# Performance work log

Hardware: AMD Instinct MI355X
Metric: run time of the kernel (lower is better)

Reference implementation:

```python
import jax, jax.numpy as jnp
import numpy as np

N_NODES = 100000
N_EDGES = 1600000
IN_DIM = 128
HID = 64
OUT_DIM = 1


def setup_inputs() -> dict:
    key = jax.random.key(0)
    ks = jax.random.split(key, 8)
    x = jax.random.normal(ks[0], (N_NODES, IN_DIM), dtype=jnp.float32)
    edge_index = jax.random.randint(ks[1], (2, N_EDGES), 0, N_NODES, dtype=jnp.int64)
    s_in = 1.0 / np.sqrt(IN_DIM)
    s_h = 1.0 / np.sqrt(HID)
    W_in = jax.random.uniform(ks[2], (IN_DIM, HID), jnp.float32, -s_in, s_in)
    b_in = jax.random.uniform(ks[3], (HID,), jnp.float32, -s_in, s_in)
    W_g = jax.random.uniform(ks[4], (HID, HID), jnp.float32, -s_h, s_h)
    b_g = jnp.zeros((HID,), jnp.float32)
    W_out = jax.random.uniform(ks[5], (HID, OUT_DIM), jnp.float32, -s_h, s_h)
    b_out = jax.random.uniform(ks[6], (OUT_DIM,), jnp.float32, -s_h, s_h)
    return {"x": x, "edge_index": edge_index, "W_in": W_in, "b_in": b_in,
            "W_g": W_g, "b_g": b_g, "W_out": W_out, "b_out": b_out}


def _gcn_conv(h, src, dst, W, b, n_nodes):
    # GCNConv: add self-loops, symmetric normalization, sum aggregation
    loops = jnp.arange(n_nodes, dtype=src.dtype)
    src = jnp.concatenate([src, loops])
    dst = jnp.concatenate([dst, loops])
    hw = h @ W  # [N, out]
    deg = jax.ops.segment_sum(jnp.ones_like(dst, dtype=hw.dtype), dst,
                              num_segments=n_nodes)  # >=1 due to self-loops
    dinv = jax.lax.rsqrt(deg)
    norm = dinv[src] * dinv[dst]  # [E+N]
    msg = hw[src] * norm[:, None]  # gather (memory-bound)
    out = jax.ops.segment_sum(msg, dst, num_segments=n_nodes)  # scatter-add
    return out + b


def reference(x, edge_index, W_in, b_in, W_g, b_g, W_out, b_out):
    n_nodes = x.shape[0]
    h = jax.nn.relu(x @ W_in + b_in)  # input_proj + ReLU (dropout = id in eval)
    # single GCN layer (last layer -> no ReLU/dropout after)
    h = _gcn_conv(h, edge_index[0], edge_index[1], W_g, b_g, n_nodes)
    return h @ W_out + b_out  # [N, 1]
```

## Files before the change

kernel.cpp:

```cpp
#include <hip/hip_runtime.h>

typedef __attribute__((ext_vector_type(8))) short bf16x8;
typedef __attribute__((ext_vector_type(4))) float f32x4;

#define HID 64
#define IN_DIM 128
#define WINB 15
#define WIN (1 << WINB)
#define NGC 4
#define MCH 64
#define SCAN_TPB 1024
#define AWORDS 32768
#define MCH2 64
#define PREP_BLOCKS 8
#define DNODES 64

__device__ __forceinline__ unsigned short f2bf(float f) {
    unsigned u = __builtin_bit_cast(unsigned, f);
    return (unsigned short)((u + 0x7FFFu + ((u >> 16) & 1u)) >> 16);
}

__global__ __launch_bounds__(SCAN_TPB) void k_binA(const int* __restrict__ dst,
                                                   unsigned* __restrict__ partA,
                                                   const float* __restrict__ W_in,
                                                   unsigned short* __restrict__ Wt,
                                                   int E, int chunkA) {
    if ((int)blockIdx.x >= MCH2) {
        int i = (blockIdx.x - MCH2) * SCAN_TPB + threadIdx.x;
        if (i < IN_DIM * HID) Wt[i] = f2bf(W_in[(i & 127) * HID + (i >> 7)]);
        return;
    }

    __shared__ unsigned cnt[AWORDS];
    for (int i = threadIdx.x; i < AWORDS; i += SCAN_TPB) cnt[i] = 0;
    __syncthreads();

    const int e0 = blockIdx.x * chunkA;
    const int e1 = min(E, e0 + chunkA);
    for (int e = e0 + (int)threadIdx.x * 4; e + 3 < e1; e += SCAN_TPB * 4) {
        int4 d4 = *(const int4*)(dst + e);
        atomicAdd(&cnt[(unsigned)d4.x >> 2], 1u << (((unsigned)d4.x & 3u) << 3));
        atomicAdd(&cnt[(unsigned)d4.y >> 2], 1u << (((unsigned)d4.y & 3u) << 3));
        atomicAdd(&cnt[(unsigned)d4.z >> 2], 1u << (((unsigned)d4.z & 3u) << 3));
        atomicAdd(&cnt[(unsigned)d4.w >> 2], 1u << (((unsigned)d4.w & 3u) << 3));
    }
    __syncthreads();

    unsigned* outp = partA + (size_t)blockIdx.x * AWORDS;
    for (int i = threadIdx.x; i < AWORDS; i += SCAN_TPB) outp[i] = cnt[i];
}

__global__ __launch_bounds__(256) void k_dense(const float* __restrict__ x,
                                               const unsigned short* __restrict__ Wt,
                                               const float* __restrict__ b_in,
                                               const float* __restrict__ W_g,
                                               const float* __restrict__ W_out,
                                               const unsigned* __restrict__ partA,
                                               float* __restrict__ dinv,
                                               float* __restrict__ zs,
                                               int N) {
    __shared__ float weff_l[HID];
    __shared__ float bl[HID];
    __shared__ float zp[DNODES];
    __shared__ int   tailp[4][DNODES];

    const int t = threadIdx.x;
    const int row0 = blockIdx.x * DNODES;

    unsigned tw[16];
    int tail_sh;
    {
        const int tn = t & 63;
        const int tq = t >> 6;
        int n = row0 + tn; if (n >= N) n = N - 1;
        tail_sh = (n & 3) << 3;
        const unsigned* base = partA + (n >> 2);
#pragma unroll
        for (int j = 0; j < 16; ++j)
            tw[j] = base[(size_t)(tq * 16 + j) * AWORDS];
    }

    {
        const float* wg = W_g + (t >> 2) * HID + (t & 3) * 16;
        const float* wo = W_out + (t & 3) * 16;
        float s = 0.0f;
#pragma unroll
        for (int p = 0; p < 16; ++p) s = fmaf(wg[p], wo[p], s);
        s += __shfl_xor(s, 1, 64);
        s += __shfl_xor(s, 2, 64);
        if ((t & 3) == 0) weff_l[t >> 2] = s;
        if (t < HID) bl[t] = b_in[t];
    }

    const int w    = __builtin_amdgcn_readfirstlane(t >> 6);
    const int lane = t & 63;

    f32x4 acc[4] = {{0,0,0,0},{0,0,0,0},{0,0,0,0},{0,0,0,0}};
    {
        int grow = row0 + w * 16 + (lane & 15);
        if (grow >= N) grow = N - 1;
        const float* xr = x + (size_t)grow * IN_DIM + (lane >> 4) * 8;
        const unsigned short* wtb = Wt + (size_t)(lane & 15) * IN_DIM + (lane >> 4) * 8;
#pragma unroll
        for (int kk = 0; kk < 4; ++kk) {
            float4 a0 = *(const float4*)(xr + kk * 32);
            float4 a1 = *(const float4*)(xr + kk * 32 + 4);
            bf16x8 af;
            af[0] = (short)f2bf(a0.x); af[1] = (short)f2bf(a0.y);
            af[2] = (short)f2bf(a0.z); af[3] = (short)f2bf(a0.w);
            af[4] = (short)f2bf(a1.x); af[5] = (short)f2bf(a1.y);
            af[6] = (short)f2bf(a1.z); af[7] = (short)f2bf(a1.w);
#pragma unroll
            for (int nf = 0; nf < 4; ++nf) {
                bf16x8 bf = *(const bf16x8*)(wtb + (size_t)(nf * 16) * IN_DIM + kk * 32);
                acc[nf] = __builtin_amdgcn_mfma_f32_16x16x32_bf16(af, bf, acc[nf], 0, 0, 0);
            }
        }
    }
    __syncthreads();

    {
        float p[4] = {0.f, 0.f, 0.f, 0.f};
#pragma unroll
        for (int nf = 0; nf < 4; ++nf) {
            const int col = nf * 16 + (lane & 15);
            const float bc = bl[col], wc = weff_l[col];
#pragma unroll
            for (int r = 0; r < 4; ++r)
                p[r] = fmaf(fmaxf(acc[nf][r] + bc, 0.0f), wc, p[r]);
        }
#pragma unroll
        for (int r = 0; r < 4; ++r) {
            p[r] += __shfl_xor(p[r], 1, 64);
            p[r] += __shfl_xor(p[r], 2, 64);
            p[r] += __shfl_xor(p[r], 4, 64);
            p[r] += __shfl_xor(p[r], 8, 64);
        }
        if ((lane & 15) == 0) {
#pragma unroll
            for (int r = 0; r < 4; ++r)
                zp[w * 16 + (lane >> 4) * 4 + r] = p[r];
        }
    }

    {
        int d = 0;
#pragma unroll
        for (int j = 0; j < 16; ++j)
            d += (int)((tw[j] >> tail_sh) & 0xFFu);
        tailp[t >> 6][t & 63] = d;
    }
    __syncthreads();

    if (t < 64) {
        int n = row0 + t; if (n >= N) n = N - 1;
        int d = tailp[0][t] + tailp[1][t] + tailp[2][t] + tailp[3][t];
        float di = rsqrtf((float)d + 1.0f);
        dinv[n] = di;
        zs[n]   = zp[t] * di;
    }
}

__global__ __launch_bounds__(SCAN_TPB) void k_binC(const int* __restrict__ eidx,
                                                   const float* __restrict__ zs,
                                                   float* __restrict__ partf,
                                                   int E, int chunk) {
    __shared__ float acc[WIN];
    for (int i = threadIdx.x; i < WIN; i += SCAN_TPB) acc[i] = 0.0f;
    __syncthreads();

    const int g = blockIdx.x % NGC;
    const int lo = g << WINB;
    const int e0 = (blockIdx.x / NGC) * chunk;
    const int e1 = min(E, e0 + chunk);
    for (int e = e0 + (int)threadIdx.x * 4; e + 3 < e1; e += SCAN_TPB * 4) {
        int4 s4 = *(const int4*)(eidx + e);
        int4 d4 = *(const int4*)(eidx + E + e);
        unsigned v;
        v = (unsigned)(d4.x - lo); if (v < WIN) atomicAdd(&acc[v], zs[s4.x]);
        v = (unsigned)(d4.y - lo); if (v < WIN) atomicAdd(&acc[v], zs[s4.y]);
        v = (unsigned)(d4.z - lo); if (v < WIN) atomicAdd(&acc[v], zs[s4.z]);
        v = (unsigned)(d4.w - lo); if (v < WIN) atomicAdd(&acc[v], zs[s4.w]);
    }
    __syncthreads();

    float* outp = partf + (size_t)blockIdx.x * WIN;
    for (int i = threadIdx.x; i < WIN; i += SCAN_TPB) outp[i] = acc[i];
}

__global__ __launch_bounds__(256) void k_redFinal(const float* __restrict__ partf,
                                                  const float* __restrict__ dinv,
                                                  const float* __restrict__ zs,
                                                  const float* __restrict__ b_g,
                                                  const float* __restrict__ W_out,
                                                  const float* __restrict__ b_out,
                                                  float* __restrict__ out, int N) {
    const int lane = threadIdx.x & 63;
    float c = b_g[lane] * W_out[lane];
#pragma unroll
    for (int off = 32; off > 0; off >>= 1)
        c += __shfl_xor(c, off, 64);
    c += b_out[0];

    int i4 = (blockIdx.x * blockDim.x + threadIdx.x) * 4;
    if (i4 >= N) return;
    const int g = i4 >> WINB, idx = i4 & (WIN - 1);

    float4 a = *(const float4*)(zs + i4);
#pragma unroll 8
    for (int m = 0; m < MCH; ++m) {
        float4 p = *(const float4*)(partf + (((size_t)m * NGC + g) << WINB) + idx);
        a.x += p.x; a.y += p.y; a.z += p.z; a.w += p.w;
    }
    float4 dv = *(const float4*)(dinv + i4);
    float4 o;
    o.x = fmaf(dv.x, a.x, c); o.y = fmaf(dv.y, a.y, c);
    o.z = fmaf(dv.z, a.z, c); o.w = fmaf(dv.w, a.w, c);
    *(float4*)(out + i4) = o;
}


extern "C" void kernel_launch(void* const* d_in, const int* in_sizes, int n_in,
                              void* d_out, int out_size, void* d_ws, size_t ws_size,
                              hipStream_t stream) {
    const float* x     = (const float*)d_in[0];
    const int*   eidx  = (const int*)d_in[1];
    const float* W_in  = (const float*)d_in[2];
    const float* b_in  = (const float*)d_in[3];
    const float* W_g   = (const float*)d_in[4];
    const float* b_g   = (const float*)d_in[5];
    const float* W_out = (const float*)d_in[6];
    const float* b_out = (const float*)d_in[7];
    float* out = (float*)d_out;

    const int N = in_sizes[0] / IN_DIM;
    const int E = in_sizes[1] / 2;

    const int chunk  = (((E + MCH  - 1) / MCH ) + 3) & ~3;
    const int chunkA = (((E + MCH2 - 1) / MCH2) + 3) & ~3;

    const size_t partElems0 = (size_t)NGC * MCH * WIN;
    const size_t partElemsA = (size_t)MCH2 * AWORDS;
    const size_t partElems = partElems0 > partElemsA ? partElems0 : partElemsA;
    unsigned* partA = (unsigned*)d_ws;
    float*    partf = (float*)d_ws;
    float*    dinv  = (float*)d_ws + partElems;
    float*    zs    = dinv + N;
    unsigned short* Wt = (unsigned short*)(zs + N);

    const int nG = (N + DNODES - 1) / DNODES;
    k_binA<<<MCH2 + PREP_BLOCKS, SCAN_TPB, 0, stream>>>(eidx + E, partA, W_in, Wt, E, chunkA);
    k_dense<<<nG, 256, 0, stream>>>(x, Wt, b_in, W_g, W_out, partA, dinv, zs, N);
    k_binC<<<NGC * MCH, SCAN_TPB, 0, stream>>>(eidx, zs, partf, E, chunk);
    k_redFinal<<<((N + 3) / 4 + 255) / 256, 256, 0, stream>>>(partf, dinv, zs, b_g, W_out, b_out, out, N);
}
```

Baseline: 65.55 us.

## Overlap degree histogram with dense projection in one fused launch

Degree binning blocks and dense projection blocks now run in one kernel, so the histogram and the GEMM-like projection can execute at the same time. The W_in bf16 transpose moves to its own small kernel. Degree reduction and the dinv/zs scaling move to a new vectorised kernel that runs afterwards. This adds one launch and an extra z array round trip. The binning blocks now use 256 threads with a 128KB shared array, which may lower occupancy and slow the histogram.

```diff
diff --git a/kernel.cpp b/kernel.cpp
--- a/kernel.cpp
+++ b/kernel.cpp
@@ -12,7 +12,6 @@
 #define SCAN_TPB 1024
 #define AWORDS 32768
 #define MCH2 64
-#define PREP_BLOCKS 8
 #define DNODES 64
 
 __device__ __forceinline__ unsigned short f2bf(float f) {
@@ -20,65 +19,49 @@
     return (unsigned short)((u + 0x7FFFu + ((u >> 16) & 1u)) >> 16);
 }
 
-__global__ __launch_bounds__(SCAN_TPB) void k_binA(const int* __restrict__ dst,
-                                                   unsigned* __restrict__ partA,
-                                                   const float* __restrict__ W_in,
-                                                   unsigned short* __restrict__ Wt,
-                                                   int E, int chunkA) {
-    if ((int)blockIdx.x >= MCH2) {
-        int i = (blockIdx.x - MCH2) * SCAN_TPB + threadIdx.x;
-        if (i < IN_DIM * HID) Wt[i] = f2bf(W_in[(i & 127) * HID + (i >> 7)]);
-        return;
-    }
-
-    __shared__ unsigned cnt[AWORDS];
-    for (int i = threadIdx.x; i < AWORDS; i += SCAN_TPB) cnt[i] = 0;
-    __syncthreads();
-
-    const int e0 = blockIdx.x * chunkA;
-    const int e1 = min(E, e0 + chunkA);
-    for (int e = e0 + (int)threadIdx.x * 4; e + 3 < e1; e += SCAN_TPB * 4) {
-        int4 d4 = *(const int4*)(dst + e);
-        atomicAdd(&cnt[(unsigned)d4.x >> 2], 1u << (((unsigned)d4.x & 3u) << 3));
-        atomicAdd(&cnt[(unsigned)d4.y >> 2], 1u << (((unsigned)d4.y & 3u) << 3));
-        atomicAdd(&cnt[(unsigned)d4.z >> 2], 1u << (((unsigned)d4.z & 3u) << 3));
-        atomicAdd(&cnt[(unsigned)d4.w >> 2], 1u << (((unsigned)d4.w & 3u) << 3));
-    }
-    __syncthreads();
-
-    unsigned* outp = partA + (size_t)blockIdx.x * AWORDS;
-    for (int i = threadIdx.x; i < AWORDS; i += SCAN_TPB) outp[i] = cnt[i];
-}
-
-__global__ __launch_bounds__(256) void k_dense(const float* __restrict__ x,
-                                               const unsigned short* __restrict__ Wt,
+__global__ __launch_bounds__(256) void k_prep(const float* __restrict__ W_in,
+                                              unsigned short* __restrict__ Wt) {
+    int i = blockIdx.x * 256 + threadIdx.x;
+    if (i < IN_DIM * HID) Wt[i] = f2bf(W_in[(i & 127) * HID + (i >> 7)]);
+}
+
+__global__ __launch_bounds__(256) void k_fused(const float* __restrict__ x,
+                                               const int* __restrict__ dst,
                                                const float* __restrict__ b_in,
                                                const float* __restrict__ W_g,
                                                const float* __restrict__ W_out,
-                                               const unsigned* __restrict__ partA,
-                                               float* __restrict__ dinv,
-                                               float* __restrict__ zs,
-                                               int N) {
+                                               const unsigned short* __restrict__ Wt,
+                                               unsigned* __restrict__ partA,
+                                               float* __restrict__ z,
+                                               int N, int E, int chunkA) {
+    const int t = threadIdx.x;
+
+    if ((int)blockIdx.x < MCH2) {
+        __shared__ unsigned cnt[AWORDS];
+        for (int i = t; i < AWORDS; i += 256) cnt[i] = 0;
+        __syncthreads();
+
+        const int e0 = blockIdx.x * chunkA;
+        const int e1 = min(E, e0 + chunkA);
+        for (int e = e0 + t * 4; e + 3 < e1; e += 256 * 4) {
+            int4 d4 = *(const int4*)(dst + e);
+            atomicAdd(&cnt[(unsigned)d4.x >> 2], 1u << (((unsigned)d4.x & 3u) << 3));
+            atomicAdd(&cnt[(unsigned)d4.y >> 2], 1u << (((unsigned)d4.y & 3u) << 3));
+            atomicAdd(&cnt[(unsigned)d4.z >> 2], 1u << (((unsigned)d4.z & 3u) << 3));
+            atomicAdd(&cnt[(unsigned)d4.w >> 2], 1u << (((unsigned)d4.w & 3u) << 3));
+        }
+        __syncthreads();
+
+        unsigned* outp = partA + (size_t)blockIdx.x * AWORDS;
+        for (int i = t; i < AWORDS; i += 256) outp[i] = cnt[i];
+        return;
+    }
+
     __shared__ float weff_l[HID];
     __shared__ float bl[HID];
     __shared__ float zp[DNODES];
-    __shared__ int   tailp[4][DNODES];
-
-    const int t = threadIdx.x;
-    const int row0 = blockIdx.x * DNODES;
-
-    unsigned tw[16];
-    int tail_sh;
-    {
-        const int tn = t & 63;
-        const int tq = t >> 6;
-        int n = row0 + tn; if (n >= N) n = N - 1;
-        tail_sh = (n & 3) << 3;
-        const unsigned* base = partA + (n >> 2);
-#pragma unroll
-        for (int j = 0; j < 16; ++j)
-            tw[j] = base[(size_t)(tq * 16 + j) * AWORDS];
-    }
+
+    const int row0 = (blockIdx.x - MCH2) * DNODES;
 
     {
         const float* wg = W_g + (t >> 2) * HID + (t & 3) * 16;
@@ -142,23 +125,38 @@
                 zp[w * 16 + (lane >> 4) * 4 + r] = p[r];
         }
     }
-
-    {
-        int d = 0;
-#pragma unroll
-        for (int j = 0; j < 16; ++j)
-            d += (int)((tw[j] >> tail_sh) & 0xFFu);
-        tailp[t >> 6][t & 63] = d;
-    }
     __syncthreads();
 
     if (t < 64) {
         int n = row0 + t; if (n >= N) n = N - 1;
-        int d = tailp[0][t] + tailp[1][t] + tailp[2][t] + tailp[3][t];
-        float di = rsqrtf((float)d + 1.0f);
-        dinv[n] = di;
-        zs[n]   = zp[t] * di;
-    }
+        z[n] = zp[t];
+    }
+}
+
+__global__ __launch_bounds__(256) void k_dinvz(const unsigned* __restrict__ partA,
+                                               const float* __restrict__ z,
+                                               float* __restrict__ dinv,
+                                               float* __restrict__ zs, int N) {
+    int i4 = (blockIdx.x * blockDim.x + threadIdx.x) * 4;
+    if (i4 >= N) return;
+    const unsigned* base = partA + (i4 >> 2);
+    int d0 = 0, d1 = 0, d2 = 0, d3 = 0;
+#pragma unroll 8
+    for (int m = 0; m < MCH2; ++m) {
+        unsigned w = base[(size_t)m * AWORDS];
+        d0 += (int)(w & 0xFFu);
+        d1 += (int)((w >> 8) & 0xFFu);
+        d2 += (int)((w >> 16) & 0xFFu);
+        d3 += (int)((w >> 24) & 0xFFu);
+    }
+    float4 dv;
+    dv.x = rsqrtf((float)d0 + 1.0f); dv.y = rsqrtf((float)d1 + 1.0f);
+    dv.z = rsqrtf((float)d2 + 1.0f); dv.w = rsqrtf((float)d3 + 1.0f);
+    float4 zv = *(const float4*)(z + i4);
+    float4 s;
+    s.x = zv.x * dv.x; s.y = zv.y * dv.y; s.z = zv.z * dv.z; s.w = zv.w * dv.w;
+    *(float4*)(dinv + i4) = dv;
+    *(float4*)(zs + i4) = s;
 }
 
 __global__ __launch_bounds__(SCAN_TPB) void k_binC(const int* __restrict__ eidx,
@@ -244,13 +242,16 @@
     const size_t partElems = partElems0 > partElemsA ? partElems0 : partElemsA;
     unsigned* partA = (unsigned*)d_ws;
     float*    partf = (float*)d_ws;
-    float*    dinv  = (float*)d_ws + partElems;
+    float*    z     = (float*)d_ws + partElems;
+    float*    dinv  = z + N;
     float*    zs    = dinv + N;
     unsigned short* Wt = (unsigned short*)(zs + N);
 
     const int nG = (N + DNODES - 1) / DNODES;
-    k_binA<<<MCH2 + PREP_BLOCKS, SCAN_TPB, 0, stream>>>(eidx + E, partA, W_in, Wt, E, chunkA);
-    k_dense<<<nG, 256, 0, stream>>>(x, Wt, b_in, W_g, W_out, partA, dinv, zs, N);
+    k_prep<<<(IN_DIM * HID + 255) / 256, 256, 0, stream>>>(W_in, Wt);
+    k_fused<<<MCH2 + nG, 256, 0, stream>>>(x, eidx + E, b_in, W_g, W_out, Wt,
+                                           partA, z, N, E, chunkA);
+    k_dinvz<<<((N + 3) / 4 + 255) / 256, 256, 0, stream>>>(partA, z, dinv, zs, N);
     k_binC<<<NGC * MCH, SCAN_TPB, 0, stream>>>(eidx, zs, partf, E, chunk);
     k_redFinal<<<((N + 3) / 4 + 255) / 256, 256, 0, stream>>>(partf, dinv, zs, b_g, W_out, b_out, out, N);
 }
```

New measurement: 72.78 us. +11.0%, slower.
